# Performance work log

Hardware: AMD Instinct MI355X
Metric: run time of the kernel (lower is better)

The kernel has to match this reference:

```python
import jax, jax.numpy as jnp
import numpy as np

D_MODEL = 768
N_HEAD = 12
D_K = D_MODEL // N_HEAD  # 64, also d_v
B, S = 2, 2048


def setup_inputs() -> dict:
    key = jax.random.key(0)
    ks = jax.random.split(key, 8)
    scale = 1.0 / np.sqrt(D_MODEL)
    return {
        "q": jax.random.normal(ks[0], (B, S, D_MODEL), dtype=jnp.float32),
        "k": jax.random.normal(ks[1], (B, S, D_MODEL), dtype=jnp.float32),
        "v": jax.random.normal(ks[2], (B, S, D_MODEL), dtype=jnp.float32),
        "mask": jax.random.randint(ks[3], (B, 1, S, S), 0, 2, dtype=jnp.int32),
        # per-head projection weights, stacked over heads: [H, d_model, d_k]
        "Wq": jax.random.normal(ks[4], (N_HEAD, D_MODEL, D_K), dtype=jnp.float32) * scale,
        "Wk": jax.random.normal(ks[5], (N_HEAD, D_MODEL, D_K), dtype=jnp.float32) * scale,
        "Wv": jax.random.normal(ks[6], (N_HEAD, D_MODEL, D_K), dtype=jnp.float32) * scale,
        # output projection: [n_head*d_v, d_model]
        "Wo": jax.random.normal(ks[7], (N_HEAD * D_K, D_MODEL), dtype=jnp.float32) * scale,
    }


def reference(q, k, v, mask, Wq, Wk, Wv, Wo):
    # Per-head projections (batched over heads instead of a python loop)
    qh = jnp.einsum("bsd,hdk->bhsk", q, Wq)  # [B,H,S,d_k]
    kh = jnp.einsum("bsd,hdk->bhsk", k, Wk)
    vh = jnp.einsum("bsd,hdk->bhsk", v, Wv)
    # Scaled dot-product attention with full score matrix (faithful to source)
    scores = jnp.einsum("bhsk,bhtk->bhst", qh, kh) / jnp.sqrt(jnp.asarray(D_K, qh.dtype))
    scores = jnp.where(mask == 0, jnp.asarray(-1e9, scores.dtype), scores)
    attn = jax.nn.softmax(scores, axis=-1)  # [B,H,S,S]
    out = jnp.einsum("bhst,bhtk->bhsk", attn, vh)  # [B,H,S,d_k]
    # concat heads (matches torch.cat over head outputs along last dim)
    out = out.transpose(0, 2, 1, 3).reshape(out.shape[0], out.shape[2], -1)  # [B,S,H*d_k]
    return out @ Wo  # [B,S,d_model]
```

## Files before the change

### kernel.cpp

```cpp
#include <hip/hip_runtime.h>
#include <stdint.h>

#define S_LEN 2048
#define NH 12
#define DM 768
#define DK 64
#define NB 2
#define MROWS (NB * S_LEN)

typedef __attribute__((ext_vector_type(8))) short short8;
typedef __attribute__((ext_vector_type(4))) float f32x4;

__device__ __forceinline__ unsigned short bf16rne(float f) {
    union { float f; uint32_t u; } v; v.f = f;
    return (unsigned short)((v.u + 0x7FFFu + ((v.u >> 16) & 1u)) >> 16);
}
__device__ __forceinline__ float bf2f(unsigned short u) {
    return __uint_as_float(((uint32_t)u) << 16);
}

__global__ __launch_bounds__(256) void prep_kernel(
        const int* __restrict__ mask, uint32_t* __restrict__ pm,
        const float* __restrict__ Wq, const float* __restrict__ Wk,
        const float* __restrict__ Wv, const float* __restrict__ Wo,
        unsigned short* __restrict__ WqT, unsigned short* __restrict__ WkT,
        unsigned short* __restrict__ WvT, unsigned short* __restrict__ WoT) {
    const int bid = blockIdx.x, tid = threadIdx.x;
    __shared__ unsigned short tile[64 * 65];
    if (bid < 32768) {
        int t = bid * 256 + tid;
        int m = mask[t];
        unsigned long long bm = __ballot(m != 0);
        if ((tid & 63) == 0) *(unsigned long long*)(pm + (t >> 5)) = bm;
        return;
    }
    const int bid2 = bid - 32768;
    const int which = bid2 / 144;
    const int tle = bid2 - which * 144;
    const int tx = tle % 12, ty = tle / 12;
    const float* W = (which == 0) ? Wq : (which == 1) ? Wk : (which == 2) ? Wv : Wo;
    unsigned short* WT = (which == 0) ? WqT : (which == 1) ? WkT : (which == 2) ? WvT : WoT;
    if (which < 3) {
        int j = tid & 63, i0 = tid >> 6;
#pragma unroll
        for (int s = 0; s < 16; ++s) {
            int i = i0 + s * 4;
            tile[i * 65 + j] = bf16rne(W[((size_t)tx * DM + ty * 64 + i) * DK + j]);
        }
        __syncthreads();
        int kd2 = tid & 63, k0 = tid >> 6;
#pragma unroll
        for (int s = 0; s < 16; ++s) {
            int kk = k0 + s * 4;
            WT[(size_t)(tx * 64 + kk) * DM + ty * 64 + kd2] = tile[kd2 * 65 + kk];
        }
    } else {
        int j = tid & 63, i0 = tid >> 6;
#pragma unroll
        for (int s = 0; s < 16; ++s) {
            int i = i0 + s * 4;
            tile[i * 65 + j] = bf16rne(W[(size_t)(ty * 64 + i) * DM + tx * 64 + j]);
        }
        __syncthreads();
        int ii = tid & 63, j0 = tid >> 6;
#pragma unroll
        for (int s = 0; s < 16; ++s) {
            int jj = j0 + s * 4;
            WT[(size_t)(tx * 64 + jj) * DM + ty * 64 + ii] = tile[ii * 65 + jj];
        }
    }
}

__global__ __launch_bounds__(256) void proj_gemm(
        const float* __restrict__ q, const float* __restrict__ k, const float* __restrict__ v,
        const unsigned short* __restrict__ WqT, const unsigned short* __restrict__ WkT,
        const unsigned short* __restrict__ WvT,
        unsigned short* __restrict__ qh, unsigned short* __restrict__ kh,
        unsigned short* __restrict__ vhT) {
    __shared__ __align__(16) unsigned short As[128 * 40];
    __shared__ __align__(16) unsigned short Bs[128 * 32];
    const int z = blockIdx.z;
    const float* A = (z == 0) ? q : (z == 1) ? k : v;
    const unsigned short* BT = (z == 0) ? WqT : (z == 1) ? WkT : WvT;
    const int tid = threadIdx.x;
    const int lane = tid & 63, wid = tid >> 6;
    const int ww = wid & 1, wh = wid >> 1;
    const int quad = lane >> 4, l16 = lane & 15;
    const int arow = tid >> 1, ac0 = (tid & 1) * 16;
    const float* Ag = A + (size_t)(blockIdx.x * 128 + arow) * DM + ac0;
    const int lr = lane >> 2, lc = (lane & 3) * 8;
    typedef __attribute__((address_space(1))) const unsigned int* gp1;
    typedef __attribute__((address_space(3))) unsigned int* lp3;
    const unsigned short* Bg = BT + (size_t)(blockIdx.y * 128 + wid * 32 + lr) * DM + lc;
    unsigned short* Bl = &Bs[wid * 32 * 32];
    f32x4 acc[4][4] = {};
    for (int kt = 0; kt < DM; kt += 32) {
        __syncthreads();
        __builtin_amdgcn_global_load_lds((gp1)(const void*)(Bg + kt),           (lp3)(void*)Bl,             16, 0, 0);
        __builtin_amdgcn_global_load_lds((gp1)(const void*)(Bg + 16 * DM + kt), (lp3)(void*)(Bl + 16 * 32), 16, 0, 0);
        float4 x0 = *(const float4*)(Ag + kt);
        float4 x1 = *(const float4*)(Ag + kt + 4);
        float4 x2 = *(const float4*)(Ag + kt + 8);
        float4 x3 = *(const float4*)(Ag + kt + 12);
        short8 h0, h1;
        h0[0] = bf16rne(x0.x); h0[1] = bf16rne(x0.y); h0[2] = bf16rne(x0.z); h0[3] = bf16rne(x0.w);
        h0[4] = bf16rne(x1.x); h0[5] = bf16rne(x1.y); h0[6] = bf16rne(x1.z); h0[7] = bf16rne(x1.w);
        h1[0] = bf16rne(x2.x); h1[1] = bf16rne(x2.y); h1[2] = bf16rne(x2.z); h1[3] = bf16rne(x2.w);
        h1[4] = bf16rne(x3.x); h1[5] = bf16rne(x3.y); h1[6] = bf16rne(x3.z); h1[7] = bf16rne(x3.w);
        *(short8*)&As[arow * 40 + ac0] = h0;
        *(short8*)&As[arow * 40 + ac0 + 8] = h1;
        __syncthreads();
        short8 af[4], bf[4];
#pragma unroll
        for (int i = 0; i < 4; ++i) af[i] = *(const short8*)&As[(wh * 64 + i * 16 + l16) * 40 + quad * 8];
#pragma unroll
        for (int j = 0; j < 4; ++j) bf[j] = *(const short8*)&Bs[(ww * 64 + j * 16 + l16) * 32 + quad * 8];
#pragma unroll
        for (int i = 0; i < 4; ++i)
#pragma unroll
            for (int j = 0; j < 4; ++j)
                acc[i][j] = __builtin_amdgcn_mfma_f32_16x16x32_bf16(af[i], bf[j], acc[i][j], 0, 0, 0);
    }

    const int row0 = blockIdx.x * 128 + wh * 64;
    const int col0 = blockIdx.y * 128 + ww * 64;
    if (z < 2) {
        unsigned short* C = z ? kh : qh;
#pragma unroll
        for (int i = 0; i < 4; ++i)
#pragma unroll
            for (int j = 0; j < 4; ++j)
#pragma unroll
                for (int r = 0; r < 4; ++r)
                    C[(size_t)(row0 + i * 16 + quad * 4 + r) * DM + col0 + j * 16 + l16] = bf16rne(acc[i][j][r]);
    } else {
#pragma unroll
        for (int i = 0; i < 4; ++i)
#pragma unroll
            for (int j = 0; j < 4; ++j) {
                int row = row0 + i * 16 + quad * 4;
                int col = col0 + j * 16 + l16;
                int bb = row >> 11, s = row & 2047;
                int hh = col >> 6, d = col & 63;
                uint32_t lo = (uint32_t)bf16rne(acc[i][j][0]) | ((uint32_t)bf16rne(acc[i][j][1]) << 16);
                uint32_t hi = (uint32_t)bf16rne(acc[i][j][2]) | ((uint32_t)bf16rne(acc[i][j][3]) << 16);
                uint2 o = make_uint2(lo, hi);
                *(uint2*)&vhT[(size_t)((bb * NH + hh) * DK + d) * S_LEN + s] = o;
            }
    }
}

__global__ __launch_bounds__(256) void attn_kernel(
        const unsigned short* __restrict__ qh, const unsigned short* __restrict__ kh,
        const unsigned short* __restrict__ vhT, const uint32_t* __restrict__ pm,
        unsigned short* __restrict__ pob, float* __restrict__ lsb) {
    const int qt = blockIdx.x, h = blockIdx.y;
    const int b = blockIdx.z >> 1, ks = blockIdx.z & 1;
    const int tid = threadIdx.x, w = tid >> 6, lane = tid & 63;
    const int quad = lane >> 4, l16 = lane & 15;
    __shared__ __align__(16) unsigned short Ks[64 * 72];
    __shared__ __align__(16) unsigned short Vs[64 * 72];
    __shared__ __align__(16) unsigned short Ps[4][32 * 72];

    const int qrow0 = qt * 128 + w * 32;
    short8 qf[2][2];
#pragma unroll
    for (int mi = 0; mi < 2; ++mi) {
        const size_t qbase = (size_t)(b * S_LEN + qrow0 + mi * 16 + l16) * DM + h * DK;
        qf[mi][0] = *(const short8*)&qh[qbase + quad * 8];
        qf[mi][1] = *(const short8*)&qh[qbase + 32 + quad * 8];
    }
    short8 of = {};
    if (l16 == 0) {
#pragma unroll
        for (int j = 0; j < 8; ++j) of[j] = (short)0x3F80;
    }

    f32x4 out[2][4] = {};
    f32x4 outl[2] = {};

    const int srow = tid >> 2, scol = (tid & 3) << 4;
    const unsigned short* Kg = kh + (size_t)b * S_LEN * DM + h * DK;
    const unsigned short* Vg = vhT + (size_t)((b * NH + h) * DK) * S_LEN;
    const uint32_t* pmb = pm + (size_t)(b * S_LEN + qrow0 + quad * 4) * 64;
    const float SCL = 0.18033688011112042f;
    const float FM = 12.0f;
    const int kt0 = ks * (S_LEN / 2);

    for (int kt = kt0; kt < kt0 + S_LEN / 2; kt += 64) {
        __syncthreads();
        *(short8*)&Ks[srow * 72 + scol]     = *(const short8*)&Kg[(size_t)(kt + srow) * DM + scol];
        *(short8*)&Ks[srow * 72 + scol + 8] = *(const short8*)&Kg[(size_t)(kt + srow) * DM + scol + 8];
        *(short8*)&Vs[srow * 72 + scol]     = *(const short8*)&Vg[(size_t)srow * S_LEN + kt + scol];
        *(short8*)&Vs[srow * 72 + scol + 8] = *(const short8*)&Vg[(size_t)srow * S_LEN + kt + scol + 8];
        __syncthreads();

        uint2 mw[2][4];
#pragma unroll
        for (int mi = 0; mi < 2; ++mi)
#pragma unroll
            for (int r = 0; r < 4; ++r)
                mw[mi][r] = *(const uint2*)&pmb[(size_t)(mi * 16 + r) * 64 + (kt >> 5)];

#pragma unroll
        for (int cb = 0; cb < 4; ++cb) {
            short8 kf0 = *(const short8*)&Ks[(cb * 16 + l16) * 72 + quad * 8];
            short8 kf1 = *(const short8*)&Ks[(cb * 16 + l16) * 72 + 32 + quad * 8];
            const int boff = ((cb & 1) << 4) + l16;
#pragma unroll
            for (int mi = 0; mi < 2; ++mi) {
                f32x4 zz = {0.f, 0.f, 0.f, 0.f};
                zz = __builtin_amdgcn_mfma_f32_16x16x32_bf16(qf[mi][0], kf0, zz, 0, 0, 0);
                zz = __builtin_amdgcn_mfma_f32_16x16x32_bf16(qf[mi][1], kf1, zz, 0, 0, 0);
#pragma unroll
                for (int r = 0; r < 4; ++r) {
                    float e = __builtin_amdgcn_exp2f(fmaf(zz[r], SCL, -FM));
                    uint32_t mword = (cb >> 1) ? mw[mi][r].y : mw[mi][r].x;
                    int32_t mneg = __builtin_amdgcn_sbfe((int32_t)mword, boff, 1);
                    uint32_t up = (__float_as_uint(e) & (uint32_t)mneg) + 0x8000u;
                    Ps[w][(mi * 16 + quad * 4 + r) * 72 + cb * 16 + l16] = (unsigned short)(up >> 16);
                }
            }
        }

        short8 pf0[2], pf1[2];
#pragma unroll
        for (int mi = 0; mi < 2; ++mi) {
            pf0[mi] = *(const short8*)&Ps[w][(mi * 16 + l16) * 72 + quad * 8];
            pf1[mi] = *(const short8*)&Ps[w][(mi * 16 + l16) * 72 + 32 + quad * 8];
        }
#pragma unroll
        for (int cb2 = 0; cb2 < 4; ++cb2) {
            short8 vf0 = *(const short8*)&Vs[(cb2 * 16 + l16) * 72 + quad * 8];
            short8 vf1 = *(const short8*)&Vs[(cb2 * 16 + l16) * 72 + 32 + quad * 8];
#pragma unroll
            for (int mi = 0; mi < 2; ++mi) {
                out[mi][cb2] = __builtin_amdgcn_mfma_f32_16x16x32_bf16(pf0[mi], vf0, out[mi][cb2], 0, 0, 0);
                out[mi][cb2] = __builtin_amdgcn_mfma_f32_16x16x32_bf16(pf1[mi], vf1, out[mi][cb2], 0, 0, 0);
            }
        }
#pragma unroll
        for (int mi = 0; mi < 2; ++mi) {
            outl[mi] = __builtin_amdgcn_mfma_f32_16x16x32_bf16(pf0[mi], of, outl[mi], 0, 0, 0);
            outl[mi] = __builtin_amdgcn_mfma_f32_16x16x32_bf16(pf1[mi], of, outl[mi], 0, 0, 0);
        }
    }

    const int pz = b * 2 + ks;
#pragma unroll
    for (int mi = 0; mi < 2; ++mi) {
#pragma unroll
        for (int r = 0; r < 4; ++r) {
            float l = outl[mi][r];
#pragma unroll
            for (int d = 1; d < 16; d <<= 1) l += __shfl_xor(l, d);
            const int row = qrow0 + mi * 16 + quad * 4 + r;
            if (l16 == 0)
                lsb[((size_t)pz * NH + h) * S_LEN + row] = l;
#pragma unroll
            for (int cb2 = 0; cb2 < 4; ++cb2)
                pob[((size_t)pz * S_LEN + row) * DM + h * DK + cb2 * 16 + l16] = bf16rne(out[mi][cb2][r]);
        }
    }
}

__global__ __launch_bounds__(256) void out_gemm(const unsigned short* __restrict__ pob,
                                                const float* __restrict__ lsb,
                                                const unsigned short* __restrict__ WoT,
                                                float* __restrict__ C) {
    __shared__ __align__(16) unsigned short As[128 * 40];
    __shared__ __align__(16) unsigned short Bs[128 * 32];
    const int tid = threadIdx.x;
    const int lane = tid & 63, wid = tid >> 6;
    const int ww = wid & 1, wh = wid >> 1;
    const int quad = lane >> 4, l16 = lane & 15;
    const int arow = tid >> 1, ac0 = (tid & 1) * 16;
    const int m = blockIdx.x * 128 + arow;
    const int bb = m >> 11, s = m & 2047;
    const unsigned short* P0 = pob + ((size_t)(bb * 2) * S_LEN + s) * DM + ac0;
    const unsigned short* P1 = pob + ((size_t)(bb * 2 + 1) * S_LEN + s) * DM + ac0;
    const float* L0 = lsb + (size_t)(bb * 2) * NH * S_LEN + s;
    const float* L1 = lsb + (size_t)(bb * 2 + 1) * NH * S_LEN + s;
    const int lr = lane >> 2, lc = (lane & 3) * 8;
    typedef __attribute__((address_space(1))) const unsigned int* gp1;
    typedef __attribute__((address_space(3))) unsigned int* lp3;
    const unsigned short* Bg = WoT + (size_t)(blockIdx.y * 128 + wid * 32 + lr) * DM + lc;
    unsigned short* Bl = &Bs[wid * 32 * 32];
    f32x4 acc[4][4] = {};
    for (int kt = 0; kt < DM; kt += 32) {
        __syncthreads();
        __builtin_amdgcn_global_load_lds((gp1)(const void*)(Bg + kt),           (lp3)(void*)Bl,             16, 0, 0);
        __builtin_amdgcn_global_load_lds((gp1)(const void*)(Bg + 16 * DM + kt), (lp3)(void*)(Bl + 16 * 32), 16, 0, 0);
        const int h = (kt + ac0) >> 6;
        float rl = 1.f / fmaxf(L0[(size_t)h * S_LEN] + L1[(size_t)h * S_LEN], 1e-37f);
        short8 a0 = *(const short8*)(P0 + kt);
        short8 a1 = *(const short8*)(P0 + kt + 8);
        short8 c0 = *(const short8*)(P1 + kt);
        short8 c1 = *(const short8*)(P1 + kt + 8);
        short8 h0, h1;
#pragma unroll
        for (int i = 0; i < 8; ++i) {
            h0[i] = bf16rne((bf2f((unsigned short)a0[i]) + bf2f((unsigned short)c0[i])) * rl);
            h1[i] = bf16rne((bf2f((unsigned short)a1[i]) + bf2f((unsigned short)c1[i])) * rl);
        }
        *(short8*)&As[arow * 40 + ac0] = h0;
        *(short8*)&As[arow * 40 + ac0 + 8] = h1;
        __syncthreads();
        short8 af[4], bf[4];
#pragma unroll
        for (int i = 0; i < 4; ++i) af[i] = *(const short8*)&As[(wh * 64 + i * 16 + l16) * 40 + quad * 8];
#pragma unroll
        for (int j = 0; j < 4; ++j) bf[j] = *(const short8*)&Bs[(ww * 64 + j * 16 + l16) * 32 + quad * 8];
#pragma unroll
        for (int i = 0; i < 4; ++i)
#pragma unroll
            for (int j = 0; j < 4; ++j)
                acc[i][j] = __builtin_amdgcn_mfma_f32_16x16x32_bf16(af[i], bf[j], acc[i][j], 0, 0, 0);
    }
    const int row0 = blockIdx.x * 128 + wh * 64;
    const int col0 = blockIdx.y * 128 + ww * 64;
#pragma unroll
    for (int i = 0; i < 4; ++i)
#pragma unroll
        for (int j = 0; j < 4; ++j)
#pragma unroll
            for (int r = 0; r < 4; ++r)
                C[(size_t)(row0 + i * 16 + quad * 4 + r) * DM + col0 + j * 16 + l16] = acc[i][j][r];
}

extern "C" void kernel_launch(void* const* d_in, const int* in_sizes, int n_in,
                              void* d_out, int out_size, void* d_ws, size_t ws_size,
                              hipStream_t stream) {
    const float* q = (const float*)d_in[0];
    const float* k = (const float*)d_in[1];
    const float* v = (const float*)d_in[2];
    const int* mask = (const int*)d_in[3];
    const float* Wq = (const float*)d_in[4];
    const float* Wk = (const float*)d_in[5];
    const float* Wv = (const float*)d_in[6];
    const float* Wo = (const float*)d_in[7];
    float* out = (float*)d_out;

    char* ws = (char*)d_ws;
    size_t off = 0;
    auto alloc = [&](size_t bytes) {
        void* p = ws + off;
        off += (bytes + 255) & ~(size_t)255;
        return p;
    };
    const size_t MAT = (size_t)MROWS * DM * 2;
    const size_t WMAT = (size_t)DM * DM * 2;
    unsigned short* WqT = (unsigned short*)alloc(WMAT);
    unsigned short* WkT = (unsigned short*)alloc(WMAT);
    unsigned short* WvT = (unsigned short*)alloc(WMAT);
    unsigned short* WoT = (unsigned short*)alloc(WMAT);
    unsigned short* qh  = (unsigned short*)alloc(MAT);
    unsigned short* kh  = (unsigned short*)alloc(MAT);
    unsigned short* vhT = (unsigned short*)alloc(MAT);
    uint32_t* pmask     = (uint32_t*)alloc((size_t)NB * S_LEN * 64 * 4);
    unsigned short* pob = (unsigned short*)alloc((size_t)4 * S_LEN * DM * 2);
    float* lsb          = (float*)alloc((size_t)4 * NH * S_LEN * 4);

    prep_kernel<<<dim3(32768 + 576), 256, 0, stream>>>(mask, pmask, Wq, Wk, Wv, Wo, WqT, WkT, WvT, WoT);
    proj_gemm<<<dim3(32, 6, 3), 256, 0, stream>>>(q, k, v, WqT, WkT, WvT, qh, kh, vhT);
    attn_kernel<<<dim3(16, 12, 4), 256, 0, stream>>>(qh, kh, vhT, pmask, pob, lsb);
    out_gemm<<<dim3(32, 6), 256, 0, stream>>>(pob, lsb, WoT, out);
}
```

Measured before the change: 246.5 us.

## Split attention keys four ways and interleave P*V per half tile

The attention kernel now splits the key dimension into four partitions instead of two, which doubles the grid to 1536 blocks and gives more parallelism across the CUs. Within each 64-key tile, softmax probabilities are produced and consumed in 32-column halves, so the per-wave P buffer in shared memory shrinks to 32x40 and the PV MFMAs can run between exp batches. The output GEMM merges four partial outputs and row sums instead of two. In exchange it writes and reads twice as much partial-output traffic and adds more bf16 rounding of partials.

```diff
diff --git a/kernel.cpp b/kernel.cpp
--- a/kernel.cpp
+++ b/kernel.cpp
@@ -155,12 +155,12 @@
         const unsigned short* __restrict__ vhT, const uint32_t* __restrict__ pm,
         unsigned short* __restrict__ pob, float* __restrict__ lsb) {
     const int qt = blockIdx.x, h = blockIdx.y;
-    const int b = blockIdx.z >> 1, ks = blockIdx.z & 1;
+    const int b = blockIdx.z >> 2, ks = blockIdx.z & 3;
     const int tid = threadIdx.x, w = tid >> 6, lane = tid & 63;
     const int quad = lane >> 4, l16 = lane & 15;
     __shared__ __align__(16) unsigned short Ks[64 * 72];
     __shared__ __align__(16) unsigned short Vs[64 * 72];
-    __shared__ __align__(16) unsigned short Ps[4][32 * 72];
+    __shared__ __align__(16) unsigned short Ps[4][32 * 40];
 
     const int qrow0 = qt * 128 + w * 32;
     short8 qf[2][2];
@@ -185,9 +185,9 @@
     const uint32_t* pmb = pm + (size_t)(b * S_LEN + qrow0 + quad * 4) * 64;
     const float SCL = 0.18033688011112042f;
     const float FM = 12.0f;
-    const int kt0 = ks * (S_LEN / 2);
-
-    for (int kt = kt0; kt < kt0 + S_LEN / 2; kt += 64) {
+    const int kt0 = ks * (S_LEN / 4), ktE = kt0 + S_LEN / 4;
+
+    for (int kt = kt0; kt < ktE; kt += 64) {
         __syncthreads();
         *(short8*)&Ks[srow * 72 + scol]     = *(const short8*)&Kg[(size_t)(kt + srow) * DM + scol];
         *(short8*)&Ks[srow * 72 + scol + 8] = *(const short8*)&Kg[(size_t)(kt + srow) * DM + scol + 8];
@@ -203,50 +203,46 @@
                 mw[mi][r] = *(const uint2*)&pmb[(size_t)(mi * 16 + r) * 64 + (kt >> 5)];
 
 #pragma unroll
-        for (int cb = 0; cb < 4; ++cb) {
-            short8 kf0 = *(const short8*)&Ks[(cb * 16 + l16) * 72 + quad * 8];
-            short8 kf1 = *(const short8*)&Ks[(cb * 16 + l16) * 72 + 32 + quad * 8];
-            const int boff = ((cb & 1) << 4) + l16;
-#pragma unroll
-            for (int mi = 0; mi < 2; ++mi) {
-                f32x4 zz = {0.f, 0.f, 0.f, 0.f};
-                zz = __builtin_amdgcn_mfma_f32_16x16x32_bf16(qf[mi][0], kf0, zz, 0, 0, 0);
-                zz = __builtin_amdgcn_mfma_f32_16x16x32_bf16(qf[mi][1], kf1, zz, 0, 0, 0);
-#pragma unroll
-                for (int r = 0; r < 4; ++r) {
-                    float e = __builtin_amdgcn_exp2f(fmaf(zz[r], SCL, -FM));
-                    uint32_t mword = (cb >> 1) ? mw[mi][r].y : mw[mi][r].x;
-                    int32_t mneg = __builtin_amdgcn_sbfe((int32_t)mword, boff, 1);
-                    uint32_t up = (__float_as_uint(e) & (uint32_t)mneg) + 0x8000u;
-                    Ps[w][(mi * 16 + quad * 4 + r) * 72 + cb * 16 + l16] = (unsigned short)(up >> 16);
+        for (int half = 0; half < 2; ++half) {
+#pragma unroll
+            for (int cc = 0; cc < 2; ++cc) {
+                const int cb = half * 2 + cc;
+                short8 kf0 = *(const short8*)&Ks[(cb * 16 + l16) * 72 + quad * 8];
+                short8 kf1 = *(const short8*)&Ks[(cb * 16 + l16) * 72 + 32 + quad * 8];
+                const int boff = (cc << 4) + l16;
+#pragma unroll
+                for (int mi = 0; mi < 2; ++mi) {
+                    f32x4 zz = {0.f, 0.f, 0.f, 0.f};
+                    zz = __builtin_amdgcn_mfma_f32_16x16x32_bf16(qf[mi][0], kf0, zz, 0, 0, 0);
+                    zz = __builtin_amdgcn_mfma_f32_16x16x32_bf16(qf[mi][1], kf1, zz, 0, 0, 0);
+#pragma unroll
+                    for (int r = 0; r < 4; ++r) {
+                        float e = __builtin_amdgcn_exp2f(fmaf(zz[r], SCL, -FM));
+                        uint32_t mword = half ? mw[mi][r].y : mw[mi][r].x;
+                        int32_t mneg = __builtin_amdgcn_sbfe((int32_t)mword, boff, 1);
+                        uint32_t up = (__float_as_uint(e) & (uint32_t)mneg) + 0x8000u;
+                        Ps[w][(mi * 16 + quad * 4 + r) * 40 + cc * 16 + l16] = (unsigned short)(up >> 16);
+                    }
                 }
             }
-        }
-
-        short8 pf0[2], pf1[2];
-#pragma unroll
-        for (int mi = 0; mi < 2; ++mi) {
-            pf0[mi] = *(const short8*)&Ps[w][(mi * 16 + l16) * 72 + quad * 8];
-            pf1[mi] = *(const short8*)&Ps[w][(mi * 16 + l16) * 72 + 32 + quad * 8];
-        }
-#pragma unroll
-        for (int cb2 = 0; cb2 < 4; ++cb2) {
-            short8 vf0 = *(const short8*)&Vs[(cb2 * 16 + l16) * 72 + quad * 8];
-            short8 vf1 = *(const short8*)&Vs[(cb2 * 16 + l16) * 72 + 32 + quad * 8];
-#pragma unroll
-            for (int mi = 0; mi < 2; ++mi) {
-                out[mi][cb2] = __builtin_amdgcn_mfma_f32_16x16x32_bf16(pf0[mi], vf0, out[mi][cb2], 0, 0, 0);
-                out[mi][cb2] = __builtin_amdgcn_mfma_f32_16x16x32_bf16(pf1[mi], vf1, out[mi][cb2], 0, 0, 0);
+            short8 pf[2];
+#pragma unroll
+            for (int mi = 0; mi < 2; ++mi)
+                pf[mi] = *(const short8*)&Ps[w][(mi * 16 + l16) * 40 + quad * 8];
+#pragma unroll
+            for (int cb2 = 0; cb2 < 4; ++cb2) {
+                short8 vf = *(const short8*)&Vs[(cb2 * 16 + l16) * 72 + half * 32 + quad * 8];
+#pragma unroll
+                for (int mi = 0; mi < 2; ++mi)
+                    out[mi][cb2] = __builtin_amdgcn_mfma_f32_16x16x32_bf16(pf[mi], vf, out[mi][cb2], 0, 0, 0);
             }
-        }
-#pragma unroll
-        for (int mi = 0; mi < 2; ++mi) {
-            outl[mi] = __builtin_amdgcn_mfma_f32_16x16x32_bf16(pf0[mi], of, outl[mi], 0, 0, 0);
-            outl[mi] = __builtin_amdgcn_mfma_f32_16x16x32_bf16(pf1[mi], of, outl[mi], 0, 0, 0);
-        }
-    }
-
-    const int pz = b * 2 + ks;
+#pragma unroll
+            for (int mi = 0; mi < 2; ++mi)
+                outl[mi] = __builtin_amdgcn_mfma_f32_16x16x32_bf16(pf[mi], of, outl[mi], 0, 0, 0);
+        }
+    }
+
+    const int pz = b * 4 + ks;
 #pragma unroll
     for (int mi = 0; mi < 2; ++mi) {
 #pragma unroll
@@ -277,10 +273,13 @@
     const int arow = tid >> 1, ac0 = (tid & 1) * 16;
     const int m = blockIdx.x * 128 + arow;
     const int bb = m >> 11, s = m & 2047;
-    const unsigned short* P0 = pob + ((size_t)(bb * 2) * S_LEN + s) * DM + ac0;
-    const unsigned short* P1 = pob + ((size_t)(bb * 2 + 1) * S_LEN + s) * DM + ac0;
-    const float* L0 = lsb + (size_t)(bb * 2) * NH * S_LEN + s;
-    const float* L1 = lsb + (size_t)(bb * 2 + 1) * NH * S_LEN + s;
+    const unsigned short* P[4];
+    const float* L[4];
+#pragma unroll
+    for (int t = 0; t < 4; ++t) {
+        P[t] = pob + ((size_t)(bb * 4 + t) * S_LEN + s) * DM + ac0;
+        L[t] = lsb + (size_t)(bb * 4 + t) * NH * S_LEN + s;
+    }
     const int lr = lane >> 2, lc = (lane & 3) * 8;
     typedef __attribute__((address_space(1))) const unsigned int* gp1;
     typedef __attribute__((address_space(3))) unsigned int* lp3;
@@ -292,16 +291,26 @@
         __builtin_amdgcn_global_load_lds((gp1)(const void*)(Bg + kt),           (lp3)(void*)Bl,             16, 0, 0);
         __builtin_amdgcn_global_load_lds((gp1)(const void*)(Bg + 16 * DM + kt), (lp3)(void*)(Bl + 16 * 32), 16, 0, 0);
         const int h = (kt + ac0) >> 6;
-        float rl = 1.f / fmaxf(L0[(size_t)h * S_LEN] + L1[(size_t)h * S_LEN], 1e-37f);
-        short8 a0 = *(const short8*)(P0 + kt);
-        short8 a1 = *(const short8*)(P0 + kt + 8);
-        short8 c0 = *(const short8*)(P1 + kt);
-        short8 c1 = *(const short8*)(P1 + kt + 8);
+        float lsum = 1e-37f;
+#pragma unroll
+        for (int t = 0; t < 4; ++t) lsum += L[t][(size_t)h * S_LEN];
+        float rl = 1.f / lsum;
+        float fa[16] = {};
+#pragma unroll
+        for (int t = 0; t < 4; ++t) {
+            short8 a0 = *(const short8*)(P[t] + kt);
+            short8 a1 = *(const short8*)(P[t] + kt + 8);
+#pragma unroll
+            for (int i = 0; i < 8; ++i) {
+                fa[i]     += bf2f((unsigned short)a0[i]);
+                fa[8 + i] += bf2f((unsigned short)a1[i]);
+            }
+        }
         short8 h0, h1;
 #pragma unroll
         for (int i = 0; i < 8; ++i) {
-            h0[i] = bf16rne((bf2f((unsigned short)a0[i]) + bf2f((unsigned short)c0[i])) * rl);
-            h1[i] = bf16rne((bf2f((unsigned short)a1[i]) + bf2f((unsigned short)c1[i])) * rl);
+            h0[i] = bf16rne(fa[i] * rl);
+            h1[i] = bf16rne(fa[8 + i] * rl);
         }
         *(short8*)&As[arow * 40 + ac0] = h0;
         *(short8*)&As[arow * 40 + ac0 + 8] = h1;
@@ -358,11 +367,11 @@
     unsigned short* kh  = (unsigned short*)alloc(MAT);
     unsigned short* vhT = (unsigned short*)alloc(MAT);
     uint32_t* pmask     = (uint32_t*)alloc((size_t)NB * S_LEN * 64 * 4);
-    unsigned short* pob = (unsigned short*)alloc((size_t)4 * S_LEN * DM * 2);
-    float* lsb          = (float*)alloc((size_t)4 * NH * S_LEN * 4);
+    unsigned short* pob = (unsigned short*)alloc((size_t)8 * S_LEN * DM * 2);
+    float* lsb          = (float*)alloc((size_t)8 * NH * S_LEN * 4);
 
     prep_kernel<<<dim3(32768 + 576), 256, 0, stream>>>(mask, pmask, Wq, Wk, Wv, Wo, WqT, WkT, WvT, WoT);
     proj_gemm<<<dim3(32, 6, 3), 256, 0, stream>>>(q, k, v, WqT, WkT, WvT, qh, kh, vhT);
-    attn_kernel<<<dim3(16, 12, 4), 256, 0, stream>>>(qh, kh, vhT, pmask, pob, lsb);
+    attn_kernel<<<dim3(16, 12, 8), 256, 0, stream>>>(qh, kh, vhT, pmask, pob, lsb);
     out_gemm<<<dim3(32, 6), 256, 0, stream>>>(pob, lsb, WoT, out);
 }
```

Result: slower. 255.4 us (+3.6%).
